# Kernel optimization log

Measured on AMD Instinct MI355X. Metric: run time of the kernel, lower is better.

Reference implementation:

```python
import jax, jax.numpy as jnp
import numpy as np

N = 65536       # n_nodes
E = 1048576     # n_edges (avg degree 16)
IDX = 256       # index_size
DIN = 512       # gcn_input_size
DH = 512        # gcn_hidden_size
DOUT = 128      # gcn_output_size
S = 256         # sample_size


def gcn_conv(h, W, b, src, dst, n):
    # PyG GCNConv: linear, add self-loops, symmetric deg^-1/2 normalization, scatter-add.
    h = h @ W
    loop = jnp.arange(n)
    s = jnp.concatenate([src, loop])
    d = jnp.concatenate([dst, loop])
    deg = jax.ops.segment_sum(jnp.ones(s.shape[0], h.dtype), d, num_segments=n)
    inv_sqrt = jax.lax.rsqrt(deg)  # deg >= 1 due to self-loops
    norm = inv_sqrt[s] * inv_sqrt[d]
    out = jax.ops.segment_sum(h[s] * norm[:, None], d, num_segments=n)
    return out + b


def _lin_init(k, fan_in, shape):
    bound = 1.0 / np.sqrt(fan_in)
    return jax.random.uniform(k, shape, jnp.float32, -bound, bound)


def setup_inputs() -> dict:
    key = jax.random.key(0)
    ks = jax.random.split(key, 14)
    x = jax.random.normal(ks[0], (N, IDX + 768), jnp.float32)
    edge_index = jax.random.randint(ks[1], (2, E), 0, N, dtype=jnp.int64)
    return {
        "x": x,
        "W_t1": _lin_init(ks[2], IDX, (IDX, DIN)),
        "b_t1": _lin_init(ks[3], IDX, (DIN,)),
        "W_t2": _lin_init(ks[4], 768, (768, DIN)),
        "b_t2": _lin_init(ks[5], 768, (DIN,)),
        "W1": _lin_init(ks[6], DIN, (DIN, DH)),
        "b1": _lin_init(ks[7], DIN, (DH,)),
        "W2": _lin_init(ks[8], DH, (DH, DOUT)),
        "b2": _lin_init(ks[9], DH, (DOUT,)),
        "matrix": jax.random.normal(ks[10], (DOUT, DOUT), jnp.float32),
        "lin_w": _lin_init(ks[11], 1, (2,)),   # nn.Linear(1, 2) weight, squeezed
        "lin_b": _lin_init(ks[12], 1, (2,)),
        "edge_index": edge_index,
    }


def reference(x, W_t1, b_t1, W_t2, b_t2, W1, b1, W2, b2, matrix, lin_w, lin_b, edge_index):
    src, dst = edge_index[0], edge_index[1]
    # dual-input linear fusion
    h = x[:, :IDX] @ W_t1 + b_t1 + x[:, IDX:] @ W_t2 + b_t2
    h = gcn_conv(h, W1, b1, src, dst, N)
    h = jax.nn.relu(h)  # dropout is identity in eval mode
    h = gcn_conv(h, W2, b2, src, dst, N)
    # per-sample bilinear score, batched over chunks
    e = h.reshape(N // S, S, DOUT)
    scores = jnp.einsum('bid,de,bje->bij', e, matrix, e)  # [B, S, S]
    out = scores[..., None] * lin_w + lin_b               # Linear(1, 2)
    return out.reshape(-1, 2)
```

## Files before the change

### kernel.cpp

```cpp
#include <hip/hip_runtime.h>
#include <stdint.h>

#define NN 65536

typedef __attribute__((ext_vector_type(8))) short bf16x8;
typedef __attribute__((ext_vector_type(4))) float f32x4;

__device__ __forceinline__ unsigned short f2bf(float f) {
    unsigned u = __float_as_uint(f);
    u += 0x7fffu + ((u >> 16) & 1u);
    return (unsigned short)(u >> 16);
}
__device__ __forceinline__ float bf2f(unsigned short h) { return __uint_as_float(((unsigned)h) << 16); }
__device__ __forceinline__ float blo(unsigned u) { return __uint_as_float(u << 16); }
__device__ __forceinline__ float bhi(unsigned u) { return __uint_as_float(u & 0xffff0000u); }
__device__ __forceinline__ unsigned pack2(float a, float b) {
    return ((unsigned)f2bf(b) << 16) | (unsigned)f2bf(a);
}

__device__ __forceinline__ void gl_lds16(const void* g, void* l) {
    __builtin_amdgcn_global_load_lds((const __attribute__((address_space(1))) void*)g,
                                     (__attribute__((address_space(3))) void*)l, 16, 0, 0);
}

__global__ void prep_pack(const float* Wt1, const float* Wt2, const float* W1,
                          const float* W2, const float* Mtx,
                          unsigned short* Wcat, unsigned short* W1T,
                          unsigned short* W2T, unsigned short* MTh, unsigned short* MTl) {
    int i = blockIdx.x * 256 + threadIdx.x;
    if (i < 524288) {
        int k = i >> 9, j = i & 511;
        float v = (k < 256) ? Wt1[k * 512 + j] : Wt2[(k - 256) * 512 + j];
        Wcat[i] = f2bf(v);
    } else if (i < 786432) {
        int t = i - 524288; int n = t >> 9, j = t & 511;
        W1T[t] = f2bf(W1[j * 512 + n]);
    } else if (i < 851968) {
        int t = i - 786432; int n = t >> 9, j = t & 511;
        W2T[t] = f2bf(W2[j * 128 + n]);
    } else if (i < 868352) {
        int t = i - 851968; int d = t >> 7, e = t & 127;
        float m = Mtx[e * 128 + d];
        unsigned short h = f2bf(m);
        MTh[t] = h; MTl[t] = f2bf(m - bf2f(h));
    }
}

__global__ void cbias_k(const float* bt1, const float* bt2, const float* W1, float* c) {
    __shared__ float sm[256];
    int t = threadIdx.x;
    int n = blockIdx.x * 32 + (t & 31);
    int jp = t >> 5;
    float acc = 0.f;
    for (int j = jp * 64; j < jp * 64 + 64; j++)
        acc += (bt1[j] + bt2[j]) * W1[j * 512 + n];
    sm[t] = acc;
    __syncthreads();
    if (t < 32) {
        float a = 0.f;
#pragma unroll
        for (int p = 0; p < 8; p++) a += sm[p * 32 + t];
        c[blockIdx.x * 32 + t] = a;
    }
}

__global__ void count_k(const int* dst, int* cnt, int E) {
    int e = blockIdx.x * 256 + threadIdx.x;
    if (e < E) atomicAdd(&cnt[dst[e]], 1);
}
__global__ void red_k(const int* cnt, int* bsum) {
    __shared__ int sm[256];
    int tid = threadIdx.x;
    sm[tid] = cnt[blockIdx.x * 256 + tid];
    __syncthreads();
    for (int s = 128; s > 0; s >>= 1) {
        if (tid < s) sm[tid] += sm[tid + s];
        __syncthreads();
    }
    if (tid == 0) bsum[blockIdx.x] = sm[0];
}
__global__ void scanb_k(const int* bsum, int* boff) {
    __shared__ int sm[256];
    int tid = threadIdx.x;
    int v0 = bsum[tid];
    sm[tid] = v0;
    __syncthreads();
    for (int s = 1; s < 256; s <<= 1) {
        int t = sm[tid];
        if (tid >= s) t += sm[tid - s];
        __syncthreads();
        sm[tid] = t;
        __syncthreads();
    }
    boff[tid] = sm[tid] - v0;
}
__global__ void scanf_k(const int* cnt, const int* boff, int* rowptr, int* cursor, float* invs) {
    __shared__ int sm[256];
    int tid = threadIdx.x;
    int i = blockIdx.x * 256 + tid;
    int v = cnt[i];
    sm[tid] = v;
    __syncthreads();
    for (int s = 1; s < 256; s <<= 1) {
        int t = sm[tid];
        if (tid >= s) t += sm[tid - s];
        __syncthreads();
        sm[tid] = t;
        __syncthreads();
    }
    int incl = sm[tid];
    int base = boff[blockIdx.x];
    int excl = base + incl - v;
    rowptr[i] = excl;
    cursor[i] = excl;
    invs[i] = rsqrtf((float)(v + 1));
    if (i == NN - 1) rowptr[NN] = base + incl;
}
__global__ void fill_k(const int* src, const int* dst, int* cursor, int* colv, int E) {
    int e = blockIdx.x * 256 + threadIdx.x;
    if (e < E) {
        int d = dst[e];
        int p = atomicAdd(&cursor[d], 1);
        colv[p] = src[e];
    }
}

__global__ __launch_bounds__(256, 2) void gemm_bt(const unsigned short* A, const unsigned short* BT,
                                                  unsigned short* C, const float* bias,
                                                  int M, int N, int K) {
    __shared__ __align__(16) unsigned short sA[128 * 32];
    __shared__ __align__(16) unsigned short sB[128 * 32];
    int tid = threadIdx.x, wave = tid >> 6, lane = tid & 63;
    int bm = blockIdx.y * 128, bn = blockIdx.x * 128;
    int wm = (wave >> 1) * 64, wn = (wave & 1) * 64;
    f32x4 acc[4][4];
#pragma unroll
    for (int i = 0; i < 4; i++)
#pragma unroll
        for (int j = 0; j < 4; j++) acc[i][j] = (f32x4){0.f, 0.f, 0.f, 0.f};
    int sr = wave * 32 + (lane >> 2);
    int sc = (lane & 3) * 8;
    const int fr = lane & 15;
    const int fk = (lane >> 4) * 8;
    for (int k0 = 0; k0 < K; k0 += 32) {
        const unsigned short* ga = A + (size_t)(bm + sr) * K + k0 + sc;
        gl_lds16(ga, &sA[sr * 32 + sc]);
        gl_lds16(ga + (size_t)16 * K, &sA[(sr + 16) * 32 + sc]);
        const unsigned short* gb = BT + (size_t)(bn + sr) * K + k0 + sc;
        gl_lds16(gb, &sB[sr * 32 + sc]);
        gl_lds16(gb + (size_t)16 * K, &sB[(sr + 16) * 32 + sc]);
        __syncthreads();
        bf16x8 af[4], bfr[4];
#pragma unroll
        for (int i = 0; i < 4; i++) af[i] = *(const bf16x8*)&sA[(wm + i * 16 + fr) * 32 + fk];
#pragma unroll
        for (int j = 0; j < 4; j++) bfr[j] = *(const bf16x8*)&sB[(wn + j * 16 + fr) * 32 + fk];
#pragma unroll
        for (int i = 0; i < 4; i++)
#pragma unroll
            for (int j = 0; j < 4; j++)
                acc[i][j] = __builtin_amdgcn_mfma_f32_16x16x32_bf16(af[i], bfr[j], acc[i][j], 0, 0, 0);
        __syncthreads();
    }
    int rq = (lane >> 4) * 4;
#pragma unroll
    for (int i = 0; i < 4; i++)
#pragma unroll
        for (int j = 0; j < 4; j++) {
            int col = bn + wn + j * 16 + fr;
            float bb = bias ? bias[col] : 0.f;
#pragma unroll
            for (int r = 0; r < 4; r++) {
                int row = bm + wm + i * 16 + rq + r;
                C[(size_t)row * N + col] = f2bf(acc[i][j][r] + bb);
            }
        }
}

__global__ __launch_bounds__(256, 2) void gemm_f32a(const float* A, const unsigned short* BT,
                                                    unsigned short* C, const float* bias) {
    const int K = 1024, N = 512;
    __shared__ __align__(16) unsigned short sA[2][128 * 32];
    __shared__ __align__(16) unsigned short sB[2][128 * 32];
    int tid = threadIdx.x, wave = tid >> 6, lane = tid & 63;
    int b = blockIdx.x;
    int xcd = b & 7, jn = (b >> 3) & 3, tt = b >> 5;
    int bm = (tt * 8 + xcd) * 128, bn = jn * 128;
    int wm = (wave >> 1) * 64, wn = (wave & 1) * 64;
    f32x4 acc[4][4];
#pragma unroll
    for (int i = 0; i < 4; i++)
#pragma unroll
        for (int j = 0; j < 4; j++) acc[i][j] = (f32x4){0.f, 0.f, 0.f, 0.f};
    int sr = wave * 32 + (lane >> 2);
    int sc = (lane & 3) * 8;
    const int fr = lane & 15;
    const int fk = (lane >> 4) * 8;
    int ar = tid >> 3, ac = (tid & 7) * 4;
    const float* Abase = A + (size_t)(bm + ar) * K + ac;
    const unsigned short* Bbase = BT + (size_t)(bn + sr) * K + sc;
    float4 ra[4];
    auto loadA = [&](int k0) {
#pragma unroll
        for (int i = 0; i < 4; i++)
            ra[i] = *(const float4*)(Abase + (size_t)(32 * i) * K + k0);
    };
    auto stageA = [&](int buf) {
#pragma unroll
        for (int i = 0; i < 4; i++) {
            ushort4 pk;
            pk.x = f2bf(ra[i].x); pk.y = f2bf(ra[i].y); pk.z = f2bf(ra[i].z); pk.w = f2bf(ra[i].w);
            *(ushort4*)&sA[buf][(ar + 32 * i) * 32 + ac] = pk;
        }
    };
    auto stageB = [&](int buf, int k0) {
        gl_lds16(Bbase + k0, &sB[buf][sr * 32 + sc]);
        gl_lds16(Bbase + (size_t)16 * K + k0, &sB[buf][(sr + 16) * 32 + sc]);
    };
    loadA(0);
    stageB(0, 0);
    stageA(0);
    loadA(32);
    __syncthreads();
    for (int k = 0; k < 32; k++) {
        int cur = k & 1, nxt = cur ^ 1;
        if (k < 31) {
            stageB(nxt, (k + 1) * 32);
            stageA(nxt);
        }
        if (k < 30) loadA((k + 2) * 32);
        bf16x8 af[4], bfr[4];
#pragma unroll
        for (int i = 0; i < 4; i++) af[i] = *(const bf16x8*)&sA[cur][(wm + i * 16 + fr) * 32 + fk];
#pragma unroll
        for (int j = 0; j < 4; j++) bfr[j] = *(const bf16x8*)&sB[cur][(wn + j * 16 + fr) * 32 + fk];
#pragma unroll
        for (int i = 0; i < 4; i++)
#pragma unroll
            for (int j = 0; j < 4; j++)
                acc[i][j] = __builtin_amdgcn_mfma_f32_16x16x32_bf16(af[i], bfr[j], acc[i][j], 0, 0, 0);
        __syncthreads();
    }
    int rq = (lane >> 4) * 4;
#pragma unroll
    for (int i = 0; i < 4; i++)
#pragma unroll
        for (int j = 0; j < 4; j++) {
            int col = bn + wn + j * 16 + fr;
            float bb = bias[col];
#pragma unroll
            for (int r = 0; r < 4; r++) {
                int row = bm + wm + i * 16 + rq + r;
                C[(size_t)row * N + col] = f2bf(acc[i][j][r] + bb);
            }
        }
}

__global__ __launch_bounds__(256, 2) void gemm_T(const unsigned short* h2h, const unsigned short* h2l,
                                                 const unsigned short* MTh, const unsigned short* MTl,
                                                 unsigned short* Th, unsigned short* Tl) {
    __shared__ __align__(16) unsigned short sA[128 * 32];
    __shared__ __align__(16) unsigned short sB[128 * 32];
    int tid = threadIdx.x, wave = tid >> 6, lane = tid & 63;
    int bm = blockIdx.x * 128;
    int wm = (wave >> 1) * 64, wn = (wave & 1) * 64;
    f32x4 acc[4][4];
#pragma unroll
    for (int i = 0; i < 4; i++)
#pragma unroll
        for (int j = 0; j < 4; j++) acc[i][j] = (f32x4){0.f, 0.f, 0.f, 0.f};
    int sr = wave * 32 + (lane >> 2);
    int sc = (lane & 3) * 8;
    const int fr = lane & 15;
    const int fk = (lane >> 4) * 8;
    const unsigned short* APs[3] = {h2h, h2h, h2l};
    const unsigned short* BPs[3] = {MTh, MTl, MTh};
    for (int it = 0; it < 12; it++) {
        int ph = it >> 2, k0 = (it & 3) * 32;
        const unsigned short* ga = APs[ph] + (size_t)(bm + sr) * 128 + k0 + sc;
        gl_lds16(ga, &sA[sr * 32 + sc]);
        gl_lds16(ga + 16 * 128, &sA[(sr + 16) * 32 + sc]);
        const unsigned short* gb = BPs[ph] + (size_t)sr * 128 + k0 + sc;
        gl_lds16(gb, &sB[sr * 32 + sc]);
        gl_lds16(gb + 16 * 128, &sB[(sr + 16) * 32 + sc]);
        __syncthreads();
        bf16x8 af[4], bfr[4];
#pragma unroll
        for (int i = 0; i < 4; i++) af[i] = *(const bf16x8*)&sA[(wm + i * 16 + fr) * 32 + fk];
#pragma unroll
        for (int j = 0; j < 4; j++) bfr[j] = *(const bf16x8*)&sB[(wn + j * 16 + fr) * 32 + fk];
#pragma unroll
        for (int i = 0; i < 4; i++)
#pragma unroll
            for (int j = 0; j < 4; j++)
                acc[i][j] = __builtin_amdgcn_mfma_f32_16x16x32_bf16(af[i], bfr[j], acc[i][j], 0, 0, 0);
        __syncthreads();
    }
    int rq = (lane >> 4) * 4;
#pragma unroll
    for (int i = 0; i < 4; i++)
#pragma unroll
        for (int j = 0; j < 4; j++) {
            int col = wn + j * 16 + fr;
#pragma unroll
            for (int r = 0; r < 4; r++) {
                int row = bm + wm + i * 16 + rq + r;
                float v = acc[i][j][r];
                unsigned short h = f2bf(v);
                Th[(size_t)row * 128 + col] = h;
                Tl[(size_t)row * 128 + col] = f2bf(v - bf2f(h));
            }
        }
}

__global__ __launch_bounds__(256) void agg512(const unsigned short* t, const int* rowptr,
                                              const int* colv, const float* invs,
                                              const float* bias, unsigned short* outp) {
    int wave = threadIdx.x >> 6, lane = threadIdx.x & 63;
    int node = blockIdx.x * 4 + wave;
    int d0 = lane * 8;
    float acc[8] = {0.f, 0.f, 0.f, 0.f, 0.f, 0.f, 0.f, 0.f};
    int r0 = rowptr[node], r1 = rowptr[node + 1];
    int e = r0;
    for (; e + 2 <= r1; e += 2) {
        int s0 = colv[e], s1 = colv[e + 1];
        float w0 = invs[s0], w1 = invs[s1];
        uint4 v0 = *(const uint4*)&t[(size_t)s0 * 512 + d0];
        uint4 v1 = *(const uint4*)&t[(size_t)s1 * 512 + d0];
        acc[0] += w0 * blo(v0.x) + w1 * blo(v1.x);
        acc[1] += w0 * bhi(v0.x) + w1 * bhi(v1.x);
        acc[2] += w0 * blo(v0.y) + w1 * blo(v1.y);
        acc[3] += w0 * bhi(v0.y) + w1 * bhi(v1.y);
        acc[4] += w0 * blo(v0.z) + w1 * blo(v1.z);
        acc[5] += w0 * bhi(v0.z) + w1 * bhi(v1.z);
        acc[6] += w0 * blo(v0.w) + w1 * blo(v1.w);
        acc[7] += w0 * bhi(v0.w) + w1 * bhi(v1.w);
    }
    if (e < r1) {
        int s = colv[e];
        float ws = invs[s];
        uint4 v = *(const uint4*)&t[(size_t)s * 512 + d0];
        acc[0] += ws * blo(v.x); acc[1] += ws * bhi(v.x);
        acc[2] += ws * blo(v.y); acc[3] += ws * bhi(v.y);
        acc[4] += ws * blo(v.z); acc[5] += ws * bhi(v.z);
        acc[6] += ws * blo(v.w); acc[7] += ws * bhi(v.w);
    }
    float wd = invs[node], wdd = wd * wd;
    uint4 sv = *(const uint4*)&t[(size_t)node * 512 + d0];
    float sf[8] = {blo(sv.x), bhi(sv.x), blo(sv.y), bhi(sv.y), blo(sv.z), bhi(sv.z), blo(sv.w), bhi(sv.w)};
    float o[8];
#pragma unroll
    for (int k = 0; k < 8; k++) {
        float v = acc[k] * wd + sf[k] * wdd + bias[d0 + k];
        o[k] = v > 0.f ? v : 0.f;
    }
    uint4 pv;
    pv.x = pack2(o[0], o[1]); pv.y = pack2(o[2], o[3]);
    pv.z = pack2(o[4], o[5]); pv.w = pack2(o[6], o[7]);
    *(uint4*)&outp[(size_t)node * 512 + d0] = pv;
}

__global__ __launch_bounds__(256) void agg128(const unsigned short* u, const int* rowptr,
                                              const int* colv, const float* invs,
                                              const float* bias, unsigned short* h2h, unsigned short* h2l) {
    int wave = threadIdx.x >> 6, lane = threadIdx.x & 63;
    int node = blockIdx.x * 4 + wave;
    int q = lane >> 4, ql = lane & 15;
    int d0 = ql * 8;
    float acc[8] = {0.f, 0.f, 0.f, 0.f, 0.f, 0.f, 0.f, 0.f};
    int r0 = rowptr[node], r1 = rowptr[node + 1];
    for (int e = r0 + q; e < r1; e += 4) {
        int s = colv[e];
        float ws = invs[s];
        uint4 v = *(const uint4*)&u[(size_t)s * 128 + d0];
        acc[0] += ws * blo(v.x); acc[1] += ws * bhi(v.x);
        acc[2] += ws * blo(v.y); acc[3] += ws * bhi(v.y);
        acc[4] += ws * blo(v.z); acc[5] += ws * bhi(v.z);
        acc[6] += ws * blo(v.w); acc[7] += ws * bhi(v.w);
    }
#pragma unroll
    for (int k = 0; k < 8; k++) {
        acc[k] += __shfl_xor(acc[k], 16);
        acc[k] += __shfl_xor(acc[k], 32);
    }
    float wd = invs[node], wdd = wd * wd;
    uint4 sv = *(const uint4*)&u[(size_t)node * 128 + d0];
    float sf[8] = {blo(sv.x), bhi(sv.x), blo(sv.y), bhi(sv.y), blo(sv.z), bhi(sv.z), blo(sv.w), bhi(sv.w)};
    unsigned short hh[8], hl[8];
#pragma unroll
    for (int k = 0; k < 8; k++) {
        float v = acc[k] * wd + sf[k] * wdd + bias[d0 + k];
        hh[k] = f2bf(v);
        hl[k] = f2bf(v - bf2f(hh[k]));
    }
    if (q == 0) {
        uint4 ph, pl;
        ph.x = ((unsigned)hh[1] << 16) | hh[0]; ph.y = ((unsigned)hh[3] << 16) | hh[2];
        ph.z = ((unsigned)hh[5] << 16) | hh[4]; ph.w = ((unsigned)hh[7] << 16) | hh[6];
        pl.x = ((unsigned)hl[1] << 16) | hl[0]; pl.y = ((unsigned)hl[3] << 16) | hl[2];
        pl.z = ((unsigned)hl[5] << 16) | hl[4]; pl.w = ((unsigned)hl[7] << 16) | hl[6];
        *(uint4*)&h2h[(size_t)node * 128 + d0] = ph;
        *(uint4*)&h2l[(size_t)node * 128 + d0] = pl;
    }
}

__global__ __launch_bounds__(256, 2) void bilinear_k(const unsigned short* Th, const unsigned short* Tl,
                                                     const unsigned short* Eh, const float* lin_w,
                                                     const float* lin_b, float* outp) {
    int tid = threadIdx.x, wave = tid >> 6, lane = tid & 63;
    int b = blockIdx.x >> 1, half = blockIdx.x & 1;
    int fr = lane & 15, q = lane >> 4;
    int irow0 = b * 256 + half * 128 + wave * 32;
    bf16x8 Ah[2][4], Al[2][4];
#pragma unroll
    for (int it = 0; it < 2; it++)
#pragma unroll
        for (int kk = 0; kk < 4; kk++) {
            size_t off = (size_t)(irow0 + it * 16 + fr) * 128 + kk * 32 + q * 8;
            Ah[it][kk] = *(const bf16x8*)&Th[off];
            Al[it][kk] = *(const bf16x8*)&Tl[off];
        }
    float w0 = lin_w[0], w1 = lin_w[1], c0 = lin_b[0], c1 = lin_b[1];
    for (int jt = 0; jt < 16; jt++) {
        bf16x8 Bf[4];
#pragma unroll
        for (int kk = 0; kk < 4; kk++)
            Bf[kk] = *(const bf16x8*)&Eh[(size_t)(b * 256 + jt * 16 + fr) * 128 + kk * 32 + q * 8];
#pragma unroll
        for (int it = 0; it < 2; it++) {
            f32x4 acc = (f32x4){0.f, 0.f, 0.f, 0.f};
#pragma unroll
            for (int kk = 0; kk < 4; kk++) {
                acc = __builtin_amdgcn_mfma_f32_16x16x32_bf16(Ah[it][kk], Bf[kk], acc, 0, 0, 0);
                acc = __builtin_amdgcn_mfma_f32_16x16x32_bf16(Al[it][kk], Bf[kk], acc, 0, 0, 0);
            }
#pragma unroll
            for (int r = 0; r < 4; r++) {
                int iloc = half * 128 + wave * 32 + it * 16 + q * 4 + r;
                int jloc = jt * 16 + fr;
                size_t o = ((size_t)b * 65536 + (size_t)iloc * 256 + jloc) * 2;
                float s = acc[r];
                float2 ov;
                ov.x = fmaf(s, w0, c0);
                ov.y = fmaf(s, w1, c1);
                *(float2*)&outp[o] = ov;
            }
        }
    }
}

extern "C" void kernel_launch(void* const* d_in, const int* in_sizes, int n_in,
                              void* d_out, int out_size, void* d_ws, size_t ws_size,
                              hipStream_t stream) {
    const float* x   = (const float*)d_in[0];
    const float* Wt1 = (const float*)d_in[1];
    const float* bt1 = (const float*)d_in[2];
    const float* Wt2 = (const float*)d_in[3];
    const float* bt2 = (const float*)d_in[4];
    const float* W1  = (const float*)d_in[5];
    const float* b1  = (const float*)d_in[6];
    const float* W2  = (const float*)d_in[7];
    const float* b2  = (const float*)d_in[8];
    const float* Mtx = (const float*)d_in[9];
    const float* lw  = (const float*)d_in[10];
    const float* lb  = (const float*)d_in[11];
    const int*   ei  = (const int*)d_in[12];
    int E = in_sizes[12] / 2;
    const int* srcp = ei;
    const int* dstp = ei + E;

    unsigned char* p = (unsigned char*)d_ws;
    size_t off = 0;
    auto alloc = [&](size_t bytes) -> void* {
        void* r = p + off;
        off = (off + bytes + 255) & ~(size_t)255;
        return r;
    };
    int*   cnt    = (int*)alloc((size_t)NN * 4);
    int*   rowptr = (int*)alloc(((size_t)NN + 1) * 4);
    int*   cursor = (int*)alloc((size_t)NN * 4);
    float* invs   = (float*)alloc((size_t)NN * 4);
    int*   bsum   = (int*)alloc(256 * 4);
    int*   boff   = (int*)alloc(256 * 4);
    int*   colv   = (int*)alloc((size_t)E * 4);
    unsigned short* Wcat   = (unsigned short*)alloc(524288 * 2);
    unsigned short* W1T    = (unsigned short*)alloc(262144 * 2);
    unsigned short* W2T    = (unsigned short*)alloc(65536 * 2);
    unsigned short* MTh    = (unsigned short*)alloc(16384 * 2);
    unsigned short* MTl    = (unsigned short*)alloc(16384 * 2);
    float*          cbias  = (float*)alloc(512 * 4);
    unsigned short* WcombT = (unsigned short*)alloc(524288 * 2);
    unsigned short* t1     = (unsigned short*)alloc((size_t)NN * 512 * 2);
    unsigned short* h1     = (unsigned short*)alloc((size_t)NN * 512 * 2);
    unsigned short* uu     = (unsigned short*)alloc((size_t)NN * 128 * 2);
    unsigned short* Th  = t1;
    unsigned short* Tl  = t1 + (size_t)NN * 128;
    unsigned short* h2h = h1;
    unsigned short* h2l = h1 + (size_t)NN * 128;

    hipMemsetAsync(cnt, 0, (size_t)NN * 4, stream);
    prep_pack<<<3392, 256, 0, stream>>>(Wt1, Wt2, W1, W2, Mtx, Wcat, W1T, W2T, MTh, MTl);
    cbias_k<<<16, 256, 0, stream>>>(bt1, bt2, W1, cbias);
    count_k<<<(E + 255) / 256, 256, 0, stream>>>(dstp, cnt, E);
    red_k<<<256, 256, 0, stream>>>(cnt, bsum);
    scanb_k<<<1, 256, 0, stream>>>(bsum, boff);
    scanf_k<<<256, 256, 0, stream>>>(cnt, boff, rowptr, cursor, invs);
    fill_k<<<(E + 255) / 256, 256, 0, stream>>>(srcp, dstp, cursor, colv, E);
    gemm_bt<<<dim3(8, 4), 256, 0, stream>>>(W1T, Wcat, WcombT, nullptr, 512, 1024, 512);
    gemm_f32a<<<2048, 256, 0, stream>>>(x, WcombT, t1, cbias);
    agg512<<<NN / 4, 256, 0, stream>>>(t1, rowptr, colv, invs, b1, h1);
    gemm_bt<<<dim3(1, 512), 256, 0, stream>>>(h1, W2T, uu, nullptr, NN, 128, 512);
    agg128<<<NN / 4, 256, 0, stream>>>(uu, rowptr, colv, invs, b2, h2h, h2l);
    gemm_T<<<512, 256, 0, stream>>>(h2h, h2l, MTh, MTl, Th, Tl);
    bilinear_k<<<512, 256, 0, stream>>>(Th, Tl, h2h, lw, lb, (float*)d_out);
}
```

Baseline: 938.5 us.

## Stage fp32 A tiles via direct LDS loads with swizzle; unroll aggregation by four

The first GEMM now loads fp32 A tiles straight into LDS through global_load_lds with an XOR swizzle. It converts them to bf16 by truncation at fragment-read time instead of round-to-nearest conversion in registers. Double buffering is removed, so there is one LDS buffer and a sync per k-step. The agg512 edge loop is unrolled to four edges per iteration to put more gathers in flight. This saves register-staging VALU work but gives up load/compute overlap and changes rounding to truncation.

New measurement: 919.1 us. 2.1% less time.

```diff
diff --git a/kernel.cpp b/kernel.cpp
--- a/kernel.cpp
+++ b/kernel.cpp
@@ -16,6 +16,9 @@
 __device__ __forceinline__ float bhi(unsigned u) { return __uint_as_float(u & 0xffff0000u); }
 __device__ __forceinline__ unsigned pack2(float a, float b) {
     return ((unsigned)f2bf(b) << 16) | (unsigned)f2bf(a);
+}
+__device__ __forceinline__ unsigned trunc2(float x, float y) {
+    return __builtin_amdgcn_perm(__float_as_uint(y), __float_as_uint(x), 0x07060302u);
 }
 
 __device__ __forceinline__ void gl_lds16(const void* g, void* l) {
@@ -180,8 +183,8 @@
 __global__ __launch_bounds__(256, 2) void gemm_f32a(const float* A, const unsigned short* BT,
                                                     unsigned short* C, const float* bias) {
     const int K = 1024, N = 512;
-    __shared__ __align__(16) unsigned short sA[2][128 * 32];
-    __shared__ __align__(16) unsigned short sB[2][128 * 32];
+    __shared__ __align__(16) float sAf[128 * 32];
+    __shared__ __align__(16) unsigned short sB[128 * 32];
     int tid = threadIdx.x, wave = tid >> 6, lane = tid & 63;
     int b = blockIdx.x;
     int xcd = b & 7, jn = (b >> 3) & 3, tt = b >> 5;
@@ -194,46 +197,36 @@
         for (int j = 0; j < 4; j++) acc[i][j] = (f32x4){0.f, 0.f, 0.f, 0.f};
     int sr = wave * 32 + (lane >> 2);
     int sc = (lane & 3) * 8;
+    int arow = lane >> 3;
+    int achk = (lane & 7) ^ arow;
     const int fr = lane & 15;
     const int fk = (lane >> 4) * 8;
-    int ar = tid >> 3, ac = (tid & 7) * 4;
-    const float* Abase = A + (size_t)(bm + ar) * K + ac;
+    const float* Abase = A + (size_t)(bm + wave * 32 + arow) * K + achk * 4;
     const unsigned short* Bbase = BT + (size_t)(bn + sr) * K + sc;
-    float4 ra[4];
-    auto loadA = [&](int k0) {
+    for (int k0 = 0; k0 < K; k0 += 32) {
 #pragma unroll
         for (int i = 0; i < 4; i++)
-            ra[i] = *(const float4*)(Abase + (size_t)(32 * i) * K + k0);
-    };
-    auto stageA = [&](int buf) {
+            gl_lds16(Abase + (size_t)(8 * i) * K + k0, &sAf[(wave * 32 + i * 8) * 32]);
+        gl_lds16(Bbase + k0, &sB[sr * 32 + sc]);
+        gl_lds16(Bbase + (size_t)16 * K + k0, &sB[(sr + 16) * 32 + sc]);
+        __syncthreads();
+        bf16x8 af[4], bfr[4];
 #pragma unroll
         for (int i = 0; i < 4; i++) {
-            ushort4 pk;
-            pk.x = f2bf(ra[i].x); pk.y = f2bf(ra[i].y); pk.z = f2bf(ra[i].z); pk.w = f2bf(ra[i].w);
-            *(ushort4*)&sA[buf][(ar + 32 * i) * 32 + ac] = pk;
+            int r = wm + i * 16 + fr;
+            int s = r & 7;
+            int c0 = fk >> 2;
+            float4 fa = *(const float4*)&sAf[r * 32 + ((c0 ^ s) << 2)];
+            float4 fb = *(const float4*)&sAf[r * 32 + (((c0 + 1) ^ s) << 2)];
+            union { unsigned u[4]; bf16x8 v; } t;
+            t.u[0] = trunc2(fa.x, fa.y);
+            t.u[1] = trunc2(fa.z, fa.w);
+            t.u[2] = trunc2(fb.x, fb.y);
+            t.u[3] = trunc2(fb.z, fb.w);
+            af[i] = t.v;
         }
-    };
-    auto stageB = [&](int buf, int k0) {
-        gl_lds16(Bbase + k0, &sB[buf][sr * 32 + sc]);
-        gl_lds16(Bbase + (size_t)16 * K + k0, &sB[buf][(sr + 16) * 32 + sc]);
-    };
-    loadA(0);
-    stageB(0, 0);
-    stageA(0);
-    loadA(32);
-    __syncthreads();
-    for (int k = 0; k < 32; k++) {
-        int cur = k & 1, nxt = cur ^ 1;
-        if (k < 31) {
-            stageB(nxt, (k + 1) * 32);
-            stageA(nxt);
-        }
-        if (k < 30) loadA((k + 2) * 32);
-        bf16x8 af[4], bfr[4];
-#pragma unroll
-        for (int i = 0; i < 4; i++) af[i] = *(const bf16x8*)&sA[cur][(wm + i * 16 + fr) * 32 + fk];
-#pragma unroll
-        for (int j = 0; j < 4; j++) bfr[j] = *(const bf16x8*)&sB[cur][(wn + j * 16 + fr) * 32 + fk];
+#pragma unroll
+        for (int j = 0; j < 4; j++) bfr[j] = *(const bf16x8*)&sB[(wn + j * 16 + fr) * 32 + fk];
 #pragma unroll
         for (int i = 0; i < 4; i++)
 #pragma unroll
@@ -322,21 +315,23 @@
     float acc[8] = {0.f, 0.f, 0.f, 0.f, 0.f, 0.f, 0.f, 0.f};
     int r0 = rowptr[node], r1 = rowptr[node + 1];
     int e = r0;
-    for (; e + 2 <= r1; e += 2) {
-        int s0 = colv[e], s1 = colv[e + 1];
-        float w0 = invs[s0], w1 = invs[s1];
+    for (; e + 4 <= r1; e += 4) {
+        int s0 = colv[e], s1 = colv[e + 1], s2 = colv[e + 2], s3 = colv[e + 3];
+        float w0 = invs[s0], w1 = invs[s1], w2 = invs[s2], w3 = invs[s3];
         uint4 v0 = *(const uint4*)&t[(size_t)s0 * 512 + d0];
         uint4 v1 = *(const uint4*)&t[(size_t)s1 * 512 + d0];
-        acc[0] += w0 * blo(v0.x) + w1 * blo(v1.x);
-        acc[1] += w0 * bhi(v0.x) + w1 * bhi(v1.x);
-        acc[2] += w0 * blo(v0.y) + w1 * blo(v1.y);
-        acc[3] += w0 * bhi(v0.y) + w1 * bhi(v1.y);
-        acc[4] += w0 * blo(v0.z) + w1 * blo(v1.z);
-        acc[5] += w0 * bhi(v0.z) + w1 * bhi(v1.z);
-        acc[6] += w0 * blo(v0.w) + w1 * blo(v1.w);
-        acc[7] += w0 * bhi(v0.w) + w1 * bhi(v1.w);
-    }
-    if (e < r1) {
+        uint4 v2 = *(const uint4*)&t[(size_t)s2 * 512 + d0];
+        uint4 v3 = *(const uint4*)&t[(size_t)s3 * 512 + d0];
+        acc[0] += w0 * blo(v0.x) + w1 * blo(v1.x) + w2 * blo(v2.x) + w3 * blo(v3.x);
+        acc[1] += w0 * bhi(v0.x) + w1 * bhi(v1.x) + w2 * bhi(v2.x) + w3 * bhi(v3.x);
+        acc[2] += w0 * blo(v0.y) + w1 * blo(v1.y) + w2 * blo(v2.y) + w3 * blo(v3.y);
+        acc[3] += w0 * bhi(v0.y) + w1 * bhi(v1.y) + w2 * bhi(v2.y) + w3 * bhi(v3.y);
+        acc[4] += w0 * blo(v0.z) + w1 * blo(v1.z) + w2 * blo(v2.z) + w3 * blo(v3.z);
+        acc[5] += w0 * bhi(v0.z) + w1 * bhi(v1.z) + w2 * bhi(v2.z) + w3 * bhi(v3.z);
+        acc[6] += w0 * blo(v0.w) + w1 * blo(v1.w) + w2 * blo(v2.w) + w3 * blo(v3.w);
+        acc[7] += w0 * bhi(v0.w) + w1 * bhi(v1.w) + w2 * bhi(v2.w) + w3 * bhi(v3.w);
+    }
+    for (; e < r1; e++) {
         int s = colv[e];
         float ws = invs[s];
         uint4 v = *(const uint4*)&t[(size_t)s * 512 + d0];
```
